# Optimization experiments

Measured on AMD Instinct MI355X. Metric: run time of the kernel, lower is better.

## Reference

```python
import jax, jax.numpy as jnp
import numpy as np
import math

B, DG, P, DA = 512, 1024, 1024, 256
LN_EPS = 1e-5  # torch LayerNorm default
EPS = 1e-12


def _ln(x, g, b):
    mu = jnp.mean(x, axis=-1, keepdims=True)
    var = jnp.mean((x - mu) ** 2, axis=-1, keepdims=True)
    return (x - mu) * jax.lax.rsqrt(var + LN_EPS) * g + b


def setup_inputs() -> dict:
    key = jax.random.key(0)
    ks = jax.random.split(key, 16)
    s = lambda fan_in: 1.0 / math.sqrt(fan_in)
    return {
        "hg": jax.random.normal(ks[0], (B, DG), jnp.float32),
        "desc_2d": jax.random.normal(ks[1], (B, P), jnp.float32),
        "Wq": jax.random.uniform(ks[2], (DA, DG), jnp.float32, -s(DG), s(DG)),
        "bq": jnp.zeros((DA,), jnp.float32),
        "wk_val": jax.random.uniform(ks[3], (DA,), jnp.float32, -1.0, 1.0),
        "bk_val": jax.random.uniform(ks[4], (DA,), jnp.float32, -1.0, 1.0),
        "wv_val": jax.random.uniform(ks[5], (DA,), jnp.float32, -1.0, 1.0),
        "bv_val": jax.random.uniform(ks[6], (DA,), jnp.float32, -1.0, 1.0),
        "Ek": jax.random.normal(ks[7], (P, DA), jnp.float32),
        "Ev": jax.random.normal(ks[8], (P, DA), jnp.float32),
        "Uq": jax.random.uniform(ks[9], (DA, DA), jnp.float32, -s(DA), s(DA)),
        "Vk": jax.random.uniform(ks[10], (DA, DA), jnp.float32, -s(DA), s(DA)),
        "ln_q_g": jnp.ones((DA,), jnp.float32), "ln_q_b": jnp.zeros((DA,), jnp.float32),
        "ln_k_g": jnp.ones((DA,), jnp.float32), "ln_k_b": jnp.zeros((DA,), jnp.float32),
        "ln_v_g": jnp.ones((DA,), jnp.float32), "ln_v_b": jnp.zeros((DA,), jnp.float32),
    }


def reference(hg, desc_2d, Wq, bq, wk_val, bk_val, wv_val, bv_val, Ek, Ev, Uq, Vk,
              ln_q_g, ln_q_b, ln_k_g, ln_k_b, ln_v_g, ln_v_b):
    # dropout is inference-mode (identity)
    q = _ln(hg @ Wq.T + bq, ln_q_g, ln_q_b)                       # (B, DA)
    # scalar -> token proj plus id embedding
    k = desc_2d[:, :, None] * wk_val + bk_val + Ek[None]          # (B, P, DA)
    v = desc_2d[:, :, None] * wv_val + bv_val + Ev[None]
    k = _ln(k, ln_k_g, ln_k_b)
    v = _ln(v, ln_v_g, ln_v_b)
    q2 = q @ Uq.T                                                 # (B, DA)
    k2 = jnp.einsum('bpd,ed->bpe', k, Vk)                         # (B, P, DA)
    e = jnp.einsum('bpd,bd->bp', k2, q2) / math.sqrt(DA)          # (B, P)
    alpha = jax.nn.sigmoid(e)
    alpha = alpha / (jnp.sum(alpha, axis=1, keepdims=True) + EPS)
    c = jnp.einsum('bp,bpd->bd', alpha, v)                        # (B, DA)
    return c, alpha
```

## Files before the change

### kernel.cpp

```cpp
#include <hip/hip_runtime.h>
#include <math.h>

#define B 512
#define DG 1024
#define P 1024
#define DA 256
#define LDP 68
#define BP (B * P)
#define BD (B * DA)

__device__ __forceinline__ float block_reduce_sum(float v, volatile float* red) {
    #pragma unroll
    for (int off = 32; off > 0; off >>= 1) v += __shfl_down(v, off, 64);
    const int lane = threadIdx.x & 63, wid = threadIdx.x >> 6;
    __syncthreads();
    if (lane == 0) red[wid] = v;
    __syncthreads();
    return red[0] + red[1] + red[2] + red[3];
}

__device__ __forceinline__ float wsum(float v) {
    #pragma unroll
    for (int m = 32; m > 0; m >>= 1) v += __shfl_xor(v, m, 64);
    return v;
}
__device__ __forceinline__ float txsum(float v) {
    #pragma unroll
    for (int m = 8; m > 0; m >>= 1) v += __shfl_xor(v, m, 16);
    return v;
}

#define FMA16(a4, b4, acc)                                   \
    acc[0][0] = fmaf(a4.x, b4.x, acc[0][0]);                 \
    acc[0][1] = fmaf(a4.x, b4.y, acc[0][1]);                 \
    acc[0][2] = fmaf(a4.x, b4.z, acc[0][2]);                 \
    acc[0][3] = fmaf(a4.x, b4.w, acc[0][3]);                 \
    acc[1][0] = fmaf(a4.y, b4.x, acc[1][0]);                 \
    acc[1][1] = fmaf(a4.y, b4.y, acc[1][1]);                 \
    acc[1][2] = fmaf(a4.y, b4.z, acc[1][2]);                 \
    acc[1][3] = fmaf(a4.y, b4.w, acc[1][3]);                 \
    acc[2][0] = fmaf(a4.z, b4.x, acc[2][0]);                 \
    acc[2][1] = fmaf(a4.z, b4.y, acc[2][1]);                 \
    acc[2][2] = fmaf(a4.z, b4.z, acc[2][2]);                 \
    acc[2][3] = fmaf(a4.z, b4.w, acc[2][3]);                 \
    acc[3][0] = fmaf(a4.w, b4.x, acc[3][0]);                 \
    acc[3][1] = fmaf(a4.w, b4.y, acc[3][1]);                 \
    acc[3][2] = fmaf(a4.w, b4.z, acc[3][2]);                 \
    acc[3][3] = fmaf(a4.w, b4.w, acc[3][3]);

#define FMA8(a0, a1, b4, acc)                                \
    acc[0][0] = fmaf(a0, b4.x, acc[0][0]);                   \
    acc[0][1] = fmaf(a0, b4.y, acc[0][1]);                   \
    acc[0][2] = fmaf(a0, b4.z, acc[0][2]);                   \
    acc[0][3] = fmaf(a0, b4.w, acc[0][3]);                   \
    acc[1][0] = fmaf(a1, b4.x, acc[1][0]);                   \
    acc[1][1] = fmaf(a1, b4.y, acc[1][1]);                   \
    acc[1][2] = fmaf(a1, b4.z, acc[1][2]);                   \
    acc[1][3] = fmaf(a1, b4.w, acc[1][3]);

__device__ __forceinline__ void stage_T(const float* __restrict__ src, int ldk, int m0, int k0,
                                        int tid, float* sD) {
    const int m = tid >> 3, k4 = (tid & 7) * 4;
    #pragma unroll
    for (int pass = 0; pass < 2; ++pass) {
        int mm = m + pass * 32;
        float4 v = *reinterpret_cast<const float4*>(&src[(m0 + mm) * ldk + k0 + k4]);
        sD[(k4 + 0) * LDP + mm] = v.x; sD[(k4 + 1) * LDP + mm] = v.y;
        sD[(k4 + 2) * LDP + mm] = v.z; sD[(k4 + 3) * LDP + mm] = v.w;
    }
}
__device__ __forceinline__ void stage_T32(const float* __restrict__ src, int ldk, int m0, int k0,
                                          int tid, float* sD) {
    const int m = tid >> 3, k4 = (tid & 7) * 4;
    float4 v = *reinterpret_cast<const float4*>(&src[(m0 + m) * ldk + k0 + k4]);
    sD[(k4 + 0) * LDP + m] = v.x; sD[(k4 + 1) * LDP + m] = v.y;
    sD[(k4 + 2) * LDP + m] = v.z; sD[(k4 + 3) * LDP + m] = v.w;
}
__device__ __forceinline__ void stage_N1(const float* __restrict__ src, int ldn, int k0, int n0,
                                         int tid, float* sD) {
    const int k = tid >> 4, n4 = (tid & 15) * 4;
    #pragma unroll
    for (int pass = 0; pass < 2; ++pass) {
        int kk = k + pass * 16;
        *reinterpret_cast<float4*>(&sD[kk * LDP + n4]) =
            *reinterpret_cast<const float4*>(&src[(k0 + kk) * ldn + n0 + n4]);
    }
}
__device__ __forceinline__ void stage_N4(const float* __restrict__ src, int pstride, int ldn,
                                         int k0, int n0, int tid, float* sD) {
    const int k = tid >> 4, n4 = (tid & 15) * 4;
    #pragma unroll
    for (int pass = 0; pass < 2; ++pass) {
        int kk = k + pass * 16;
        const float* base = &src[(k0 + kk) * ldn + n0 + n4];
        float4 v = *reinterpret_cast<const float4*>(base);
        #pragma unroll
        for (int s = 1; s < 4; ++s) {
            float4 w = *reinterpret_cast<const float4*>(base + s * pstride);
            v.x += w.x; v.y += w.y; v.z += w.z; v.w += w.w;
        }
        *reinterpret_cast<float4*>(&sD[kk * LDP + n4]) = v;
    }
}
__device__ __forceinline__ void mm_inner(const float* sA, const float* sB, int tid, float acc[4][4]) {
    const int ty4 = (tid >> 4) * 4, tx4 = (tid & 15) * 4;
    #pragma unroll
    for (int kk = 0; kk < 32; ++kk) {
        float4 a4 = *reinterpret_cast<const float4*>(&sA[kk * LDP + ty4]);
        float4 b4 = *reinterpret_cast<const float4*>(&sB[kk * LDP + tx4]);
        FMA16(a4, b4, acc)
    }
}

__global__ __launch_bounds__(256) void KA(const float* __restrict__ hg, const float* __restrict__ Wq,
                                          const float* __restrict__ Uq, const float* __restrict__ Vk,
                                          const float* __restrict__ Ek, const float* __restrict__ Ev,
                                          const float* __restrict__ wk, const float* __restrict__ bk,
                                          const float* __restrict__ wv, const float* __restrict__ bv,
                                          const float* __restrict__ gk, const float* __restrict__ bkln,
                                          float* __restrict__ qp, float* __restrict__ Gp,
                                          float* __restrict__ UqT, float* __restrict__ Sacc,
                                          float* __restrict__ pst, float* __restrict__ scal4,
                                          float* __restrict__ vec4) {
    __shared__ __align__(16) float sA[32 * LDP];
    __shared__ __align__(16) float sB[32 * LDP];
    const int tid = threadIdx.x;
    const int t = blockIdx.x;
    const int ty4 = (tid >> 4) * 4, tx4 = (tid & 15) * 4;

    if (t < 256) {
        const int mt = t & 7, nt = (t >> 3) & 3, ks = t >> 5;
        const int b0 = mt * 64, d0 = nt * 64, kc = ks * 128;
        float acc[4][4] = {};
        for (int kt = 0; kt < 128; kt += 32) {
            stage_T(hg, DG, b0, kc + kt, tid, sA);
            stage_T(Wq, DG, d0, kc + kt, tid, sB);
            __syncthreads();
            mm_inner(sA, sB, tid, acc);
            __syncthreads();
        }
        float* outp = qp + ks * BD;
        #pragma unroll
        for (int i = 0; i < 4; ++i) {
            float4 o = make_float4(acc[i][0], acc[i][1], acc[i][2], acc[i][3]);
            *reinterpret_cast<float4*>(&outp[(b0 + ty4 + i) * DA + d0 + tx4]) = o;
        }
    } else if (t < 512) {
        const int t2 = t - 256;
        const int et = t2 & 3, pt = (t2 >> 2) & 15, ks = t2 >> 6;
        const int e0 = et * 64, p0 = pt * 64, kc = ks * 64;
        float acc[4][4] = {};
        for (int kt = 0; kt < 64; kt += 32) {
            const int kg = kc + kt;
            {
                const int m = tid >> 3, k4 = (tid & 7) * 4;
                float4 g = *reinterpret_cast<const float4*>(&gk[kg + k4]);
                #pragma unroll
                for (int pass = 0; pass < 2; ++pass) {
                    int mm = m + pass * 32;
                    float4 v = *reinterpret_cast<const float4*>(&Vk[(e0 + mm) * DA + kg + k4]);
                    sA[(k4 + 0) * LDP + mm] = v.x * g.x; sA[(k4 + 1) * LDP + mm] = v.y * g.y;
                    sA[(k4 + 2) * LDP + mm] = v.z * g.z; sA[(k4 + 3) * LDP + mm] = v.w * g.w;
                }
            }
            stage_T(Ek, DA, p0, kg, tid, sB);
            __syncthreads();
            mm_inner(sA, sB, tid, acc);
            __syncthreads();
        }
        float* outp = Gp + ks * (DA * P);
        #pragma unroll
        for (int i = 0; i < 4; ++i) {
            float4 o = make_float4(acc[i][0], acc[i][1], acc[i][2], acc[i][3]);
            *reinterpret_cast<float4*>(&outp[(e0 + ty4 + i) * P + p0 + tx4]) = o;
        }
    } else if (t < 576) {
        const int b2 = t - 512;
        const int e0 = (b2 & 7) * 32, f0 = (b2 >> 3) * 32;
        const int col = tid & 31, row8 = tid >> 5;
        #pragma unroll
        for (int pass = 0; pass < 4; ++pass) {
            int r = row8 + pass * 8;
            sA[r * 33 + col] = Uq[(e0 + r) * DA + f0 + col];
        }
        __syncthreads();
        #pragma unroll
        for (int pass = 0; pass < 4; ++pass) {
            int r = row8 + pass * 8;
            UqT[(f0 + r) * DA + e0 + col] = sA[col * 33 + r];
        }
    } else if (t == 576) {
        #pragma unroll
        for (int j = 0; j < 8; ++j) Sacc[j * 256 + tid] = 0.f;
        float* w4  = sA;
        float* tmp = sB;
        float gkd = gk[tid];
        w4[0 * 256 + tid] = wk[tid] * gkd;
        w4[1 * 256 + tid] = bk[tid] * gkd;
        w4[2 * 256 + tid] = gkd;
        w4[3 * 256 + tid] = bkln[tid];
        __syncthreads();
        const int dl = tid & 15, eg = tid >> 4;
        for (int eb = 0; eb < 16; ++eb) {
            int e = eb * 16 + eg;
            float p0 = 0.f, p1 = 0.f, p2 = 0.f, p3 = 0.f;
            #pragma unroll
            for (int tt = 0; tt < 16; ++tt) {
                int d = dl + tt * 16;
                float v = Vk[e * DA + d];
                p0 = fmaf(v, w4[d], p0);
                p1 = fmaf(v, w4[256 + d], p1);
                p2 = fmaf(v, w4[512 + d], p2);
                p3 = fmaf(v, w4[768 + d], p3);
            }
            #pragma unroll
            for (int m = 8; m > 0; m >>= 1) {
                p0 += __shfl_xor(p0, m, 16);
                p1 += __shfl_xor(p1, m, 16);
                p2 += __shfl_xor(p2, m, 16);
                p3 += __shfl_xor(p3, m, 16);
            }
            if (dl == 0) {
                tmp[e * 4 + 0] = p0; tmp[e * 4 + 1] = p1;
                tmp[e * 4 + 2] = p2; tmp[e * 4 + 3] = p3;
            }
        }
        __syncthreads();
        float a0 = 0.f, a1 = 0.f, a2 = 0.f, a3 = 0.f;
        for (int e = 0; e < 256; ++e) {
            float u = Uq[e * DA + tid];
            a0 = fmaf(u, tmp[e * 4 + 0], a0);
            a1 = fmaf(u, tmp[e * 4 + 1], a1);
            a2 = fmaf(u, tmp[e * 4 + 2], a2);
            a3 = fmaf(u, tmp[e * 4 + 3], a3);
        }
        vec4[tid] = a0; vec4[256 + tid] = a1; vec4[512 + tid] = a2; vec4[768 + tid] = a3;
    } else {
        const int tp = t - 577;
        const int wid = tid >> 6, lane = tid & 63;
        const int p = tp * 4 + wid;
        const int d4 = lane * 4;
        const float inv = 1.0f / DA;
        float4 ek4 = *reinterpret_cast<const float4*>(&Ek[p * DA + d4]);
        float4 ev4 = *reinterpret_cast<const float4*>(&Ev[p * DA + d4]);
        float4 wk4 = *reinterpret_cast<const float4*>(&wk[d4]);
        float4 bk4 = *reinterpret_cast<const float4*>(&bk[d4]);
        float4 wv4 = *reinterpret_cast<const float4*>(&wv[d4]);
        float4 bv4 = *reinterpret_cast<const float4*>(&bv[d4]);
        float ck0 = bk4.x + ek4.x, ck1 = bk4.y + ek4.y, ck2 = bk4.z + ek4.z, ck3 = bk4.w + ek4.w;
        float cv0 = bv4.x + ev4.x, cv1 = bv4.y + ev4.y, cv2 = bv4.z + ev4.z, cv3 = bv4.w + ev4.w;
        float Sck  = wsum(ck0 + ck1 + ck2 + ck3);
        float Sck2 = wsum(ck0*ck0 + ck1*ck1 + ck2*ck2 + ck3*ck3);
        float Swck = wsum(wk4.x*ck0 + wk4.y*ck1 + wk4.z*ck2 + wk4.w*ck3);
        float Scv  = wsum(cv0 + cv1 + cv2 + cv3);
        float Scv2 = wsum(cv0*cv0 + cv1*cv1 + cv2*cv2 + cv3*cv3);
        float Swcv = wsum(wv4.x*cv0 + wv4.y*cv1 + wv4.z*cv2 + wv4.w*cv3);
        float Swk  = wsum(wk4.x + wk4.y + wk4.z + wk4.w);
        float Swv  = wsum(wv4.x + wv4.y + wv4.z + wv4.w);
        float mwk = Swk * inv, mwv = Swv * inv;
        float mck = Sck * inv, mcv = Scv * inv;
        if (lane == 0) {
            pst[0 * P + p] = mck;
            pst[1 * P + p] = Swck * inv - mwk * mck;
            pst[2 * P + p] = Sck2 * inv - mck * mck;
            pst[3 * P + p] = mcv;
            pst[4 * P + p] = Swcv * inv - mwv * mcv;
            pst[5 * P + p] = Scv2 * inv - mcv * mcv;
        }
        if (p == 0) {
            float Swk2 = wsum(wk4.x*wk4.x + wk4.y*wk4.y + wk4.z*wk4.z + wk4.w*wk4.w);
            float Swv2 = wsum(wv4.x*wv4.x + wv4.y*wv4.y + wv4.z*wv4.z + wv4.w*wv4.w);
            if (lane == 0) {
                scal4[0] = mwk;
                scal4[1] = Swk2 * inv - mwk * mwk;
                scal4[2] = mwv;
                scal4[3] = Swv2 * inv - mwv * mwv;
            }
        }
    }
}

__global__ __launch_bounds__(256) void KC(const float* __restrict__ qp, const float* __restrict__ bq,
                                          const float* __restrict__ gq, const float* __restrict__ bqln,
                                          const float* __restrict__ vec4, const float* __restrict__ UqT,
                                          float* __restrict__ q2out, float* __restrict__ bscal) {
    __shared__ __align__(16) float q_lds[DA];
    __shared__ float red[4];
    const int b = blockIdx.x, d = threadIdx.x;
    float x = bq[d];
    #pragma unroll
    for (int ks = 0; ks < 8; ++ks) x += qp[ks * BD + b * DA + d];
    float mu = block_reduce_sum(x, red) * (1.0f / DA);
    float xc = x - mu;
    float var = block_reduce_sum(xc * xc, red) * (1.0f / DA);
    float qv = xc * rsqrtf(var + 1e-5f) * gq[d] + bqln[d];
    q_lds[d] = qv;
    float Wg = block_reduce_sum(qv * vec4[d], red);
    float Cg = block_reduce_sum(qv * vec4[256 + d], red);
    float G_ = block_reduce_sum(qv * vec4[512 + d], red);
    float Bb = block_reduce_sum(qv * vec4[768 + d], red);
    if (d == 0) {
        bscal[b] = Wg; bscal[B + b] = Cg;
        bscal[2 * B + b] = G_; bscal[3 * B + b] = Bb;
    }
    float q2 = 0.f;
    for (int f = 0; f < DA; f += 4) {
        float4 qf = *reinterpret_cast<const float4*>(&q_lds[f]);
        q2 = fmaf(qf.x, UqT[(f + 0) * DA + d], q2);
        q2 = fmaf(qf.y, UqT[(f + 1) * DA + d], q2);
        q2 = fmaf(qf.z, UqT[(f + 2) * DA + d], q2);
        q2 = fmaf(qf.w, UqT[(f + 3) * DA + d], q2);
    }
    q2out[b * DA + d] = q2;
}

__global__ __launch_bounds__(256) void KD(const float* __restrict__ q2, const float* __restrict__ Gp,
                                          const float* __restrict__ desc, const float* __restrict__ bscal,
                                          const float* __restrict__ pst, const float* __restrict__ scal4,
                                          float* __restrict__ ubuf, float* __restrict__ wbuf,
                                          float* __restrict__ Sacc) {
    __shared__ __align__(16) float sA[32 * LDP];
    __shared__ __align__(16) float sB[32 * LDP];
    const int tid = threadIdx.x, t = blockIdx.x;
    const int tx = tid & 15, ty = tid >> 4;
    const int tx4 = tx * 4;
    const int b0 = (t & 15) * 32, p0 = (t >> 4) * 64;
    float acc[2][4] = {};
    for (int kt = 0; kt < 256; kt += 32) {
        stage_T32(q2, DA, b0, kt, tid, sA);
        stage_N4(Gp, DA * P, P, kt, p0, tid, sB);
        __syncthreads();
        #pragma unroll
        for (int kk = 0; kk < 32; ++kk) {
            float a0 = sA[kk * LDP + ty * 2 + 0];
            float a1 = sA[kk * LDP + ty * 2 + 1];
            float4 b4 = *reinterpret_cast<const float4*>(&sB[kk * LDP + tx4]);
            FMA8(a0, a1, b4, acc)
        }
        __syncthreads();
    }
    const float mwk = scal4[0], Ak = scal4[1], mwv = scal4[2], Av = scal4[3];
    #pragma unroll
    for (int i = 0; i < 2; ++i) {
        const int b = b0 + ty * 2 + i;
        const float Wg = bscal[b], Cg = bscal[B + b], G_ = bscal[2 * B + b], Bb = bscal[3 * B + b];
        float4 uo, wo;
        float* up = &uo.x; float* wp = &wo.x;
        float us = 0.f, ws_ = 0.f, wss = 0.f, wms = 0.f;
        #pragma unroll
        for (int j = 0; j < 4; ++j) {
            const int p = p0 + tx4 + j;
            float s = desc[b * P + p];
            float mck = pst[p], Bk = pst[P + p], Ck = pst[2 * P + p];
            float var = fmaf(s, fmaf(s, Ak, 2.0f * Bk), Ck);
            float rstd = rsqrtf(var + 1e-5f);
            float mu = fmaf(s, mwk, mck);
            float e = (rstd * (fmaf(s, Wg, Cg) + acc[i][j] - mu * G_) + Bb) * 0.0625f;
            float uu = 1.0f / (1.0f + expf(-e));
            float mcv = pst[3 * P + p], Bv = pst[4 * P + p], Cv = pst[5 * P + p];
            float varv = fmaf(s, fmaf(s, Av, 2.0f * Bv), Cv);
            float rv = rsqrtf(varv + 1e-5f);
            float ww = uu * rv;
            up[j] = uu; wp[j] = ww;
            us += uu; ws_ += ww;
            wss = fmaf(ww, s, wss);
            wms = fmaf(ww, fmaf(s, mwv, mcv), wms);
        }
        *reinterpret_cast<float4*>(&ubuf[b * P + p0 + tx4]) = uo;
        *reinterpret_cast<float4*>(&wbuf[b * P + p0 + tx4]) = wo;
        us = txsum(us); ws_ = txsum(ws_); wss = txsum(wss); wms = txsum(wms);
        if (tx == 0) {
            atomicAdd(&Sacc[b], us);
            atomicAdd(&Sacc[B + b], ws_);
            atomicAdd(&Sacc[2 * B + b], wss);
            atomicAdd(&Sacc[3 * B + b], wms);
        }
    }
}

__global__ __launch_bounds__(256) void KF(const float* __restrict__ wbuf, const float* __restrict__ Ev,
                                          float* __restrict__ cpart) {
    __shared__ __align__(16) float sA[32 * LDP];
    __shared__ __align__(16) float sB[32 * LDP];
    const int tid = threadIdx.x, t = blockIdx.x;
    const int ty4 = (tid >> 4) * 4, tx4 = (tid & 15) * 4;
    const int mt = t & 7, nt = (t >> 3) & 3, ks = t >> 5;
    const int b0 = mt * 64, d0 = nt * 64, kc = ks * 128;
    float acc[4][4] = {};
    for (int kt = 0; kt < 128; kt += 32) {
        stage_T(wbuf, P, b0, kc + kt, tid, sA);
        stage_N1(Ev, DA, kc + kt, d0, tid, sB);
        __syncthreads();
        mm_inner(sA, sB, tid, acc);
        __syncthreads();
    }
    float* outp = cpart + ks * BD;
    #pragma unroll
    for (int i = 0; i < 4; ++i) {
        float4 o = make_float4(acc[i][0], acc[i][1], acc[i][2], acc[i][3]);
        *reinterpret_cast<float4*>(&outp[(b0 + ty4 + i) * DA + d0 + tx4]) = o;
    }
}

__global__ __launch_bounds__(256) void KG(const float* __restrict__ cpart, const float* __restrict__ Sacc,
                                          const float* __restrict__ ubuf,
                                          const float* __restrict__ gv, const float* __restrict__ wv,
                                          const float* __restrict__ bvv, const float* __restrict__ bvln,
                                          float* __restrict__ alpha_out, float* __restrict__ out_c) {
    const int b = blockIdx.x, tid = threadIdx.x;
    const float S = Sacc[b], SB = Sacc[B + b], SBs = Sacc[2 * B + b], SBm = Sacc[3 * B + b];
    const float invS = 1.0f / (S + 1e-12f);
    const float T = S * invS;
    #pragma unroll
    for (int j = 0; j < 4; ++j) {
        int p = j * 256 + tid;
        alpha_out[b * P + p] = ubuf[b * P + p] * invS;
    }
    const int d = tid;
    float csum = 0.f;
    #pragma unroll
    for (int ks = 0; ks < 8; ++ks) csum += cpart[ks * BD + b * DA + d];
    out_c[b * DA + d] =
        invS * (gv[d] * (wv[d] * SBs + bvv[d] * SB + csum - SBm)) + bvln[d] * T;
}

extern "C" void kernel_launch(void* const* d_in, const int* in_sizes, int n_in,
                              void* d_out, int out_size, void* d_ws, size_t ws_size,
                              hipStream_t stream) {
    (void)in_sizes; (void)n_in; (void)out_size; (void)ws_size;
    const float* hg   = (const float*)d_in[0];
    const float* desc = (const float*)d_in[1];
    const float* Wq   = (const float*)d_in[2];
    const float* bq   = (const float*)d_in[3];
    const float* wk   = (const float*)d_in[4];
    const float* bk   = (const float*)d_in[5];
    const float* wv   = (const float*)d_in[6];
    const float* bv   = (const float*)d_in[7];
    const float* Ek   = (const float*)d_in[8];
    const float* Ev   = (const float*)d_in[9];
    const float* Uq   = (const float*)d_in[10];
    const float* Vk   = (const float*)d_in[11];
    const float* gq   = (const float*)d_in[12];
    const float* bqln = (const float*)d_in[13];
    const float* gk   = (const float*)d_in[14];
    const float* bkln = (const float*)d_in[15];
    const float* gv   = (const float*)d_in[16];
    const float* bvln = (const float*)d_in[17];

    float* out = (float*)d_out;
    float* out_c = out;
    float* out_alpha = out + BD;

    float* ws = (float*)d_ws;
    float* qp    = ws;
    float* Gp    = ws + 1048576;
    float* UqT   = ws + 2097152;
    float* q2    = ws + 2162688;
    float* ubuf  = ws + 2293760;
    float* wbuf  = ws + 2818048;
    float* cpart = ws + 3342336;
    float* vec4  = ws + 4390912;
    float* bscal = ws + 4391936;
    float* Sacc  = ws + 4393984;
    float* pst   = ws + 4396032;
    float* scal4 = ws + 4402176;

    KA<<<833, 256, 0, stream>>>(hg, Wq, Uq, Vk, Ek, Ev, wk, bk, wv, bv, gk, bkln,
                                qp, Gp, UqT, Sacc, pst, scal4, vec4);
    KC<<<512, 256, 0, stream>>>(qp, bq, gq, bqln, vec4, UqT, q2, bscal);
    KD<<<256, 256, 0, stream>>>(q2, Gp, desc, bscal, pst, scal4, ubuf, wbuf, Sacc);
    KF<<<256, 256, 0, stream>>>(wbuf, Ev, cpart);
    KG<<<512, 256, 0, stream>>>(cpart, Sacc, ubuf, gv, wv, bv, bvln, out_alpha, out_c);
}
```

Baseline: 70.31 us.

## Split-K the score GEMM, add per-row epilogue kernel, drop atomics

The Gp partials are reduced from four to two K-splits in KA. The score GEMM in KD becomes a 64x64-tiled split-K over four partial buffers instead of a 32-row tile with a fused sigmoid epilogue and atomics. A new per-row kernel KE sums the partials, applies the sigmoid and LayerNorm statistics, reduces the row sums in-block, and writes alpha and the bias part of c. KF now splits K into 16 chunks to raise block count, and KG only adds the GEMM term. This removes the Sacc zeroing and atomics and raises parallelism, at the cost of an extra launch and more partial-buffer traffic.

```diff
diff --git a/kernel.cpp b/kernel.cpp
--- a/kernel.cpp
+++ b/kernel.cpp
@@ -18,15 +18,9 @@
     __syncthreads();
     return red[0] + red[1] + red[2] + red[3];
 }
-
 __device__ __forceinline__ float wsum(float v) {
     #pragma unroll
     for (int m = 32; m > 0; m >>= 1) v += __shfl_xor(v, m, 64);
-    return v;
-}
-__device__ __forceinline__ float txsum(float v) {
-    #pragma unroll
-    for (int m = 8; m > 0; m >>= 1) v += __shfl_xor(v, m, 16);
     return v;
 }
 
@@ -48,16 +42,6 @@
     acc[3][2] = fmaf(a4.w, b4.z, acc[3][2]);                 \
     acc[3][3] = fmaf(a4.w, b4.w, acc[3][3]);
 
-#define FMA8(a0, a1, b4, acc)                                \
-    acc[0][0] = fmaf(a0, b4.x, acc[0][0]);                   \
-    acc[0][1] = fmaf(a0, b4.y, acc[0][1]);                   \
-    acc[0][2] = fmaf(a0, b4.z, acc[0][2]);                   \
-    acc[0][3] = fmaf(a0, b4.w, acc[0][3]);                   \
-    acc[1][0] = fmaf(a1, b4.x, acc[1][0]);                   \
-    acc[1][1] = fmaf(a1, b4.y, acc[1][1]);                   \
-    acc[1][2] = fmaf(a1, b4.z, acc[1][2]);                   \
-    acc[1][3] = fmaf(a1, b4.w, acc[1][3]);
-
 __device__ __forceinline__ void stage_T(const float* __restrict__ src, int ldk, int m0, int k0,
                                         int tid, float* sD) {
     const int m = tid >> 3, k4 = (tid & 7) * 4;
@@ -69,13 +53,6 @@
         sD[(k4 + 2) * LDP + mm] = v.z; sD[(k4 + 3) * LDP + mm] = v.w;
     }
 }
-__device__ __forceinline__ void stage_T32(const float* __restrict__ src, int ldk, int m0, int k0,
-                                          int tid, float* sD) {
-    const int m = tid >> 3, k4 = (tid & 7) * 4;
-    float4 v = *reinterpret_cast<const float4*>(&src[(m0 + m) * ldk + k0 + k4]);
-    sD[(k4 + 0) * LDP + m] = v.x; sD[(k4 + 1) * LDP + m] = v.y;
-    sD[(k4 + 2) * LDP + m] = v.z; sD[(k4 + 3) * LDP + m] = v.w;
-}
 __device__ __forceinline__ void stage_N1(const float* __restrict__ src, int ldn, int k0, int n0,
                                          int tid, float* sD) {
     const int k = tid >> 4, n4 = (tid & 15) * 4;
@@ -86,7 +63,7 @@
             *reinterpret_cast<const float4*>(&src[(k0 + kk) * ldn + n0 + n4]);
     }
 }
-__device__ __forceinline__ void stage_N4(const float* __restrict__ src, int pstride, int ldn,
+__device__ __forceinline__ void stage_N2(const float* __restrict__ src, int pstride, int ldn,
                                          int k0, int n0, int tid, float* sD) {
     const int k = tid >> 4, n4 = (tid & 15) * 4;
     #pragma unroll
@@ -94,11 +71,8 @@
         int kk = k + pass * 16;
         const float* base = &src[(k0 + kk) * ldn + n0 + n4];
         float4 v = *reinterpret_cast<const float4*>(base);
-        #pragma unroll
-        for (int s = 1; s < 4; ++s) {
-            float4 w = *reinterpret_cast<const float4*>(base + s * pstride);
-            v.x += w.x; v.y += w.y; v.z += w.z; v.w += w.w;
-        }
+        float4 w = *reinterpret_cast<const float4*>(base + pstride);
+        v.x += w.x; v.y += w.y; v.z += w.z; v.w += w.w;
         *reinterpret_cast<float4*>(&sD[kk * LDP + n4]) = v;
     }
 }
@@ -119,13 +93,12 @@
                                           const float* __restrict__ wv, const float* __restrict__ bv,
                                           const float* __restrict__ gk, const float* __restrict__ bkln,
                                           float* __restrict__ qp, float* __restrict__ Gp,
-                                          float* __restrict__ UqT, float* __restrict__ Sacc,
+                                          float* __restrict__ UqT,
                                           float* __restrict__ pst, float* __restrict__ scal4,
                                           float* __restrict__ vec4) {
     __shared__ __align__(16) float sA[32 * LDP];
     __shared__ __align__(16) float sB[32 * LDP];
-    const int tid = threadIdx.x;
-    const int t = blockIdx.x;
+    const int tid = threadIdx.x, t = blockIdx.x;
     const int ty4 = (tid >> 4) * 4, tx4 = (tid & 15) * 4;
 
     if (t < 256) {
@@ -145,12 +118,12 @@
             float4 o = make_float4(acc[i][0], acc[i][1], acc[i][2], acc[i][3]);
             *reinterpret_cast<float4*>(&outp[(b0 + ty4 + i) * DA + d0 + tx4]) = o;
         }
-    } else if (t < 512) {
+    } else if (t < 384) {
         const int t2 = t - 256;
         const int et = t2 & 3, pt = (t2 >> 2) & 15, ks = t2 >> 6;
-        const int e0 = et * 64, p0 = pt * 64, kc = ks * 64;
+        const int e0 = et * 64, p0 = pt * 64, kc = ks * 128;
         float acc[4][4] = {};
-        for (int kt = 0; kt < 64; kt += 32) {
+        for (int kt = 0; kt < 128; kt += 32) {
             const int kg = kc + kt;
             {
                 const int m = tid >> 3, k4 = (tid & 7) * 4;
@@ -174,8 +147,8 @@
             float4 o = make_float4(acc[i][0], acc[i][1], acc[i][2], acc[i][3]);
             *reinterpret_cast<float4*>(&outp[(e0 + ty4 + i) * P + p0 + tx4]) = o;
         }
-    } else if (t < 576) {
-        const int b2 = t - 512;
+    } else if (t < 448) {
+        const int b2 = t - 384;
         const int e0 = (b2 & 7) * 32, f0 = (b2 >> 3) * 32;
         const int col = tid & 31, row8 = tid >> 5;
         #pragma unroll
@@ -189,9 +162,7 @@
             int r = row8 + pass * 8;
             UqT[(f0 + r) * DA + e0 + col] = sA[col * 33 + r];
         }
-    } else if (t == 576) {
-        #pragma unroll
-        for (int j = 0; j < 8; ++j) Sacc[j * 256 + tid] = 0.f;
+    } else if (t == 448) {
         float* w4  = sA;
         float* tmp = sB;
         float gkd = gk[tid];
@@ -236,7 +207,7 @@
         }
         vec4[tid] = a0; vec4[256 + tid] = a1; vec4[512 + tid] = a2; vec4[768 + tid] = a3;
     } else {
-        const int tp = t - 577;
+        const int tp = t - 449;
         const int wid = tid >> 6, lane = tid & 63;
         const int p = tp * 4 + wid;
         const int d4 = lane * 4;
@@ -315,67 +286,76 @@
 }
 
 __global__ __launch_bounds__(256) void KD(const float* __restrict__ q2, const float* __restrict__ Gp,
-                                          const float* __restrict__ desc, const float* __restrict__ bscal,
-                                          const float* __restrict__ pst, const float* __restrict__ scal4,
-                                          float* __restrict__ ubuf, float* __restrict__ wbuf,
-                                          float* __restrict__ Sacc) {
+                                          float* __restrict__ epart) {
     __shared__ __align__(16) float sA[32 * LDP];
     __shared__ __align__(16) float sB[32 * LDP];
     const int tid = threadIdx.x, t = blockIdx.x;
-    const int tx = tid & 15, ty = tid >> 4;
-    const int tx4 = tx * 4;
-    const int b0 = (t & 15) * 32, p0 = (t >> 4) * 64;
-    float acc[2][4] = {};
-    for (int kt = 0; kt < 256; kt += 32) {
-        stage_T32(q2, DA, b0, kt, tid, sA);
-        stage_N4(Gp, DA * P, P, kt, p0, tid, sB);
-        __syncthreads();
-        #pragma unroll
-        for (int kk = 0; kk < 32; ++kk) {
-            float a0 = sA[kk * LDP + ty * 2 + 0];
-            float a1 = sA[kk * LDP + ty * 2 + 1];
-            float4 b4 = *reinterpret_cast<const float4*>(&sB[kk * LDP + tx4]);
-            FMA8(a0, a1, b4, acc)
-        }
-        __syncthreads();
-    }
+    const int ty4 = (tid >> 4) * 4, tx4 = (tid & 15) * 4;
+    const int bt = t & 7, pt = (t >> 3) & 15, ks = t >> 7;
+    const int b0 = bt * 64, p0 = pt * 64, kc = ks * 64;
+    float acc[4][4] = {};
+    for (int kt = 0; kt < 64; kt += 32) {
+        stage_T(q2, DA, b0, kc + kt, tid, sA);
+        stage_N2(Gp, DA * P, P, kc + kt, p0, tid, sB);
+        __syncthreads();
+        mm_inner(sA, sB, tid, acc);
+        __syncthreads();
+    }
+    float* outp = epart + ks * BP;
+    #pragma unroll
+    for (int i = 0; i < 4; ++i) {
+        float4 o = make_float4(acc[i][0], acc[i][1], acc[i][2], acc[i][3]);
+        *reinterpret_cast<float4*>(&outp[(b0 + ty4 + i) * P + p0 + tx4]) = o;
+    }
+}
+
+__global__ __launch_bounds__(256) void KE(const float* __restrict__ epart, const float* __restrict__ desc,
+                                          const float* __restrict__ bscal, const float* __restrict__ pst,
+                                          const float* __restrict__ scal4,
+                                          const float* __restrict__ gv, const float* __restrict__ wv,
+                                          const float* __restrict__ bvv, const float* __restrict__ bvln,
+                                          float* __restrict__ alpha_out, float* __restrict__ wbuf,
+                                          float* __restrict__ bscal2, float* __restrict__ out_c) {
+    __shared__ float red[4];
+    const int b = blockIdx.x, tid = threadIdx.x;
     const float mwk = scal4[0], Ak = scal4[1], mwv = scal4[2], Av = scal4[3];
-    #pragma unroll
-    for (int i = 0; i < 2; ++i) {
-        const int b = b0 + ty * 2 + i;
-        const float Wg = bscal[b], Cg = bscal[B + b], G_ = bscal[2 * B + b], Bb = bscal[3 * B + b];
-        float4 uo, wo;
-        float* up = &uo.x; float* wp = &wo.x;
-        float us = 0.f, ws_ = 0.f, wss = 0.f, wms = 0.f;
-        #pragma unroll
-        for (int j = 0; j < 4; ++j) {
-            const int p = p0 + tx4 + j;
-            float s = desc[b * P + p];
-            float mck = pst[p], Bk = pst[P + p], Ck = pst[2 * P + p];
-            float var = fmaf(s, fmaf(s, Ak, 2.0f * Bk), Ck);
-            float rstd = rsqrtf(var + 1e-5f);
-            float mu = fmaf(s, mwk, mck);
-            float e = (rstd * (fmaf(s, Wg, Cg) + acc[i][j] - mu * G_) + Bb) * 0.0625f;
-            float uu = 1.0f / (1.0f + expf(-e));
-            float mcv = pst[3 * P + p], Bv = pst[4 * P + p], Cv = pst[5 * P + p];
-            float varv = fmaf(s, fmaf(s, Av, 2.0f * Bv), Cv);
-            float rv = rsqrtf(varv + 1e-5f);
-            float ww = uu * rv;
-            up[j] = uu; wp[j] = ww;
-            us += uu; ws_ += ww;
-            wss = fmaf(ww, s, wss);
-            wms = fmaf(ww, fmaf(s, mwv, mcv), wms);
-        }
-        *reinterpret_cast<float4*>(&ubuf[b * P + p0 + tx4]) = uo;
-        *reinterpret_cast<float4*>(&wbuf[b * P + p0 + tx4]) = wo;
-        us = txsum(us); ws_ = txsum(ws_); wss = txsum(wss); wms = txsum(wms);
-        if (tx == 0) {
-            atomicAdd(&Sacc[b], us);
-            atomicAdd(&Sacc[B + b], ws_);
-            atomicAdd(&Sacc[2 * B + b], wss);
-            atomicAdd(&Sacc[3 * B + b], wms);
-        }
-    }
+    const float Wg = bscal[b], Cg = bscal[B + b], G_ = bscal[2 * B + b], Bb = bscal[3 * B + b];
+    float u[4];
+    float us = 0.f, ws_ = 0.f, wss = 0.f, wms = 0.f;
+    #pragma unroll
+    for (int j = 0; j < 4; ++j) {
+        int p = j * 256 + tid;
+        float dot = epart[b * P + p] + epart[BP + b * P + p]
+                  + epart[2 * BP + b * P + p] + epart[3 * BP + b * P + p];
+        float s = desc[b * P + p];
+        float mck = pst[p], Bk = pst[P + p], Ck = pst[2 * P + p];
+        float var = fmaf(s, fmaf(s, Ak, 2.0f * Bk), Ck);
+        float rstd = rsqrtf(var + 1e-5f);
+        float mu = fmaf(s, mwk, mck);
+        float e = (rstd * (fmaf(s, Wg, Cg) + dot - mu * G_) + Bb) * 0.0625f;
+        float uu = 1.0f / (1.0f + expf(-e));
+        float mcv = pst[3 * P + p], Bv = pst[4 * P + p], Cv = pst[5 * P + p];
+        float varv = fmaf(s, fmaf(s, Av, 2.0f * Bv), Cv);
+        float rv = rsqrtf(varv + 1e-5f);
+        float ww = uu * rv;
+        wbuf[b * P + p] = ww;
+        u[j] = uu;
+        us += uu; ws_ += ww;
+        wss = fmaf(ww, s, wss);
+        wms = fmaf(ww, fmaf(s, mwv, mcv), wms);
+    }
+    float S   = block_reduce_sum(us, red);
+    float SB  = block_reduce_sum(ws_, red);
+    float SBs = block_reduce_sum(wss, red);
+    float SBm = block_reduce_sum(wms, red);
+    float invS = 1.0f / (S + 1e-12f);
+    float T = S * invS;
+    #pragma unroll
+    for (int j = 0; j < 4; ++j)
+        alpha_out[b * P + j * 256 + tid] = u[j] * invS;
+    if (tid == 0) bscal2[b] = invS;
+    const int d = tid;
+    out_c[b * DA + d] = invS * (gv[d] * (wv[d] * SBs + bvv[d] * SB - SBm)) + bvln[d] * T;
 }
 
 __global__ __launch_bounds__(256) void KF(const float* __restrict__ wbuf, const float* __restrict__ Ev,
@@ -385,9 +365,9 @@
     const int tid = threadIdx.x, t = blockIdx.x;
     const int ty4 = (tid >> 4) * 4, tx4 = (tid & 15) * 4;
     const int mt = t & 7, nt = (t >> 3) & 3, ks = t >> 5;
-    const int b0 = mt * 64, d0 = nt * 64, kc = ks * 128;
+    const int b0 = mt * 64, d0 = nt * 64, kc = ks * 64;
     float acc[4][4] = {};
-    for (int kt = 0; kt < 128; kt += 32) {
+    for (int kt = 0; kt < 64; kt += 32) {
         stage_T(wbuf, P, b0, kc + kt, tid, sA);
         stage_N1(Ev, DA, kc + kt, d0, tid, sB);
         __syncthreads();
@@ -402,26 +382,13 @@
     }
 }
 
-__global__ __launch_bounds__(256) void KG(const float* __restrict__ cpart, const float* __restrict__ Sacc,
-                                          const float* __restrict__ ubuf,
-                                          const float* __restrict__ gv, const float* __restrict__ wv,
-                                          const float* __restrict__ bvv, const float* __restrict__ bvln,
-                                          float* __restrict__ alpha_out, float* __restrict__ out_c) {
-    const int b = blockIdx.x, tid = threadIdx.x;
-    const float S = Sacc[b], SB = Sacc[B + b], SBs = Sacc[2 * B + b], SBm = Sacc[3 * B + b];
-    const float invS = 1.0f / (S + 1e-12f);
-    const float T = S * invS;
-    #pragma unroll
-    for (int j = 0; j < 4; ++j) {
-        int p = j * 256 + tid;
-        alpha_out[b * P + p] = ubuf[b * P + p] * invS;
-    }
-    const int d = tid;
+__global__ __launch_bounds__(256) void KG(const float* __restrict__ cpart, const float* __restrict__ bscal2,
+                                          const float* __restrict__ gv, float* __restrict__ out_c) {
+    const int b = blockIdx.x, d = threadIdx.x;
     float csum = 0.f;
     #pragma unroll
-    for (int ks = 0; ks < 8; ++ks) csum += cpart[ks * BD + b * DA + d];
-    out_c[b * DA + d] =
-        invS * (gv[d] * (wv[d] * SBs + bvv[d] * SB + csum - SBm)) + bvln[d] * T;
+    for (int ks = 0; ks < 16; ++ks) csum += cpart[ks * BD + b * DA + d];
+    out_c[b * DA + d] = fmaf(bscal2[b] * gv[d], csum, out_c[b * DA + d]);
 }
 
 extern "C" void kernel_launch(void* const* d_in, const int* in_sizes, int n_in,
@@ -454,21 +421,23 @@
     float* ws = (float*)d_ws;
     float* qp    = ws;
     float* Gp    = ws + 1048576;
-    float* UqT   = ws + 2097152;
-    float* q2    = ws + 2162688;
-    float* ubuf  = ws + 2293760;
-    float* wbuf  = ws + 2818048;
-    float* cpart = ws + 3342336;
-    float* vec4  = ws + 4390912;
-    float* bscal = ws + 4391936;
-    float* Sacc  = ws + 4393984;
-    float* pst   = ws + 4396032;
-    float* scal4 = ws + 4402176;
-
-    KA<<<833, 256, 0, stream>>>(hg, Wq, Uq, Vk, Ek, Ev, wk, bk, wv, bv, gk, bkln,
-                                qp, Gp, UqT, Sacc, pst, scal4, vec4);
+    float* UqT   = ws + 1572864;
+    float* q2    = ws + 1638400;
+    float* epart = ws + 1769472;
+    float* wbuf  = ws + 3866624;
+    float* cpart = ws + 4390912;
+    float* vec4  = ws + 6488064;
+    float* bscal = ws + 6489088;
+    float* bscal2= ws + 6491136;
+    float* pst   = ws + 6491648;
+    float* scal4 = ws + 6497792;
+
+    KA<<<705, 256, 0, stream>>>(hg, Wq, Uq, Vk, Ek, Ev, wk, bk, wv, bv, gk, bkln,
+                                qp, Gp, UqT, pst, scal4, vec4);
     KC<<<512, 256, 0, stream>>>(qp, bq, gq, bqln, vec4, UqT, q2, bscal);
-    KD<<<256, 256, 0, stream>>>(q2, Gp, desc, bscal, pst, scal4, ubuf, wbuf, Sacc);
-    KF<<<256, 256, 0, stream>>>(wbuf, Ev, cpart);
-    KG<<<512, 256, 0, stream>>>(cpart, Sacc, ubuf, gv, wv, bv, bvln, out_alpha, out_c);
-}
+    KD<<<512, 256, 0, stream>>>(q2, Gp, epart);
+    KE<<<512, 256, 0, stream>>>(epart, desc, bscal, pst, scal4, gv, wv, bv, bvln,
+                                out_alpha, wbuf, bscal2, out_c);
+    KF<<<512, 256, 0, stream>>>(wbuf, Ev, cpart);
+    KG<<<512, 256, 0, stream>>>(cpart, bscal2, gv, out_c);
+}
```

New measurement: 64.05 us. 8.9% less time.

## Reassociate q·Uq·Vk·Ek via small M=Uq^T·diag(gk)Vk and fuse final reduction into KF

Applied to the files above, without the earlier changes.

Instead of precomputing G = (Vk·diag(gk))·Ek^T (DA×P, split-K partials summed in KD) and transposing Uq, the code precomputes the small DA×DA product M = Uq^T·diag(gk)·Vk in two split-K partials. KC then computes gr = q·M directly, and KD multiplies gr by Ek in place of summing four G partials. The separate KG kernel is removed: KF applies the normalisation epilogue and accumulates its split-K partials into out_c with atomicAdd (zeroed in KC), and also writes alpha. This cuts workspace traffic and one launch, at the cost of atomics and non-deterministic summation order.

```diff
diff --git a/kernel.cpp b/kernel.cpp
--- a/kernel.cpp
+++ b/kernel.cpp
@@ -18,7 +18,6 @@
     __syncthreads();
     return red[0] + red[1] + red[2] + red[3];
 }
-
 __device__ __forceinline__ float wsum(float v) {
     #pragma unroll
     for (int m = 32; m > 0; m >>= 1) v += __shfl_xor(v, m, 64);
@@ -86,22 +85,6 @@
             *reinterpret_cast<const float4*>(&src[(k0 + kk) * ldn + n0 + n4]);
     }
 }
-__device__ __forceinline__ void stage_N4(const float* __restrict__ src, int pstride, int ldn,
-                                         int k0, int n0, int tid, float* sD) {
-    const int k = tid >> 4, n4 = (tid & 15) * 4;
-    #pragma unroll
-    for (int pass = 0; pass < 2; ++pass) {
-        int kk = k + pass * 16;
-        const float* base = &src[(k0 + kk) * ldn + n0 + n4];
-        float4 v = *reinterpret_cast<const float4*>(base);
-        #pragma unroll
-        for (int s = 1; s < 4; ++s) {
-            float4 w = *reinterpret_cast<const float4*>(base + s * pstride);
-            v.x += w.x; v.y += w.y; v.z += w.z; v.w += w.w;
-        }
-        *reinterpret_cast<float4*>(&sD[kk * LDP + n4]) = v;
-    }
-}
 __device__ __forceinline__ void mm_inner(const float* sA, const float* sB, int tid, float acc[4][4]) {
     const int ty4 = (tid >> 4) * 4, tx4 = (tid & 15) * 4;
     #pragma unroll
@@ -118,14 +101,13 @@
                                           const float* __restrict__ wk, const float* __restrict__ bk,
                                           const float* __restrict__ wv, const float* __restrict__ bv,
                                           const float* __restrict__ gk, const float* __restrict__ bkln,
-                                          float* __restrict__ qp, float* __restrict__ Gp,
-                                          float* __restrict__ UqT, float* __restrict__ Sacc,
+                                          float* __restrict__ qp, float* __restrict__ Mp,
+                                          float* __restrict__ Sacc,
                                           float* __restrict__ pst, float* __restrict__ scal4,
                                           float* __restrict__ vec4) {
     __shared__ __align__(16) float sA[32 * LDP];
     __shared__ __align__(16) float sB[32 * LDP];
-    const int tid = threadIdx.x;
-    const int t = blockIdx.x;
+    const int tid = threadIdx.x, t = blockIdx.x;
     const int ty4 = (tid >> 4) * 4, tx4 = (tid & 15) * 4;
 
     if (t < 256) {
@@ -145,51 +127,34 @@
             float4 o = make_float4(acc[i][0], acc[i][1], acc[i][2], acc[i][3]);
             *reinterpret_cast<float4*>(&outp[(b0 + ty4 + i) * DA + d0 + tx4]) = o;
         }
-    } else if (t < 512) {
+    } else if (t < 288) {
         const int t2 = t - 256;
-        const int et = t2 & 3, pt = (t2 >> 2) & 15, ks = t2 >> 6;
-        const int e0 = et * 64, p0 = pt * 64, kc = ks * 64;
+        const int ft = t2 & 3, dt = (t2 >> 2) & 3, ks = t2 >> 4;
+        const int f0 = ft * 64, d0 = dt * 64, kc = ks * 128;
+        const int k = tid >> 4, n4 = (tid & 15) * 4;
         float acc[4][4] = {};
-        for (int kt = 0; kt < 64; kt += 32) {
+        for (int kt = 0; kt < 128; kt += 32) {
             const int kg = kc + kt;
-            {
-                const int m = tid >> 3, k4 = (tid & 7) * 4;
-                float4 g = *reinterpret_cast<const float4*>(&gk[kg + k4]);
-                #pragma unroll
-                for (int pass = 0; pass < 2; ++pass) {
-                    int mm = m + pass * 32;
-                    float4 v = *reinterpret_cast<const float4*>(&Vk[(e0 + mm) * DA + kg + k4]);
-                    sA[(k4 + 0) * LDP + mm] = v.x * g.x; sA[(k4 + 1) * LDP + mm] = v.y * g.y;
-                    sA[(k4 + 2) * LDP + mm] = v.z * g.z; sA[(k4 + 3) * LDP + mm] = v.w * g.w;
-                }
+            stage_N1(Uq, DA, kg, f0, tid, sA);
+            float4 g = *reinterpret_cast<const float4*>(&gk[d0 + n4]);
+            #pragma unroll
+            for (int pass = 0; pass < 2; ++pass) {
+                int kk = k + pass * 16;
+                float4 v = *reinterpret_cast<const float4*>(&Vk[(kg + kk) * DA + d0 + n4]);
+                v.x *= g.x; v.y *= g.y; v.z *= g.z; v.w *= g.w;
+                *reinterpret_cast<float4*>(&sB[kk * LDP + n4]) = v;
             }
-            stage_T(Ek, DA, p0, kg, tid, sB);
             __syncthreads();
             mm_inner(sA, sB, tid, acc);
             __syncthreads();
         }
-        float* outp = Gp + ks * (DA * P);
+        float* outp = Mp + ks * (DA * DA);
         #pragma unroll
         for (int i = 0; i < 4; ++i) {
             float4 o = make_float4(acc[i][0], acc[i][1], acc[i][2], acc[i][3]);
-            *reinterpret_cast<float4*>(&outp[(e0 + ty4 + i) * P + p0 + tx4]) = o;
-        }
-    } else if (t < 576) {
-        const int b2 = t - 512;
-        const int e0 = (b2 & 7) * 32, f0 = (b2 >> 3) * 32;
-        const int col = tid & 31, row8 = tid >> 5;
-        #pragma unroll
-        for (int pass = 0; pass < 4; ++pass) {
-            int r = row8 + pass * 8;
-            sA[r * 33 + col] = Uq[(e0 + r) * DA + f0 + col];
-        }
-        __syncthreads();
-        #pragma unroll
-        for (int pass = 0; pass < 4; ++pass) {
-            int r = row8 + pass * 8;
-            UqT[(f0 + r) * DA + e0 + col] = sA[col * 33 + r];
-        }
-    } else if (t == 576) {
+            *reinterpret_cast<float4*>(&outp[(f0 + ty4 + i) * DA + d0 + tx4]) = o;
+        }
+    } else if (t == 288) {
         #pragma unroll
         for (int j = 0; j < 8; ++j) Sacc[j * 256 + tid] = 0.f;
         float* w4  = sA;
@@ -236,7 +201,7 @@
         }
         vec4[tid] = a0; vec4[256 + tid] = a1; vec4[512 + tid] = a2; vec4[768 + tid] = a3;
     } else {
-        const int tp = t - 577;
+        const int tp = t - 289;
         const int wid = tid >> 6, lane = tid & 63;
         const int p = tp * 4 + wid;
         const int d4 = lane * 4;
@@ -282,8 +247,9 @@
 
 __global__ __launch_bounds__(256) void KC(const float* __restrict__ qp, const float* __restrict__ bq,
                                           const float* __restrict__ gq, const float* __restrict__ bqln,
-                                          const float* __restrict__ vec4, const float* __restrict__ UqT,
-                                          float* __restrict__ q2out, float* __restrict__ bscal) {
+                                          const float* __restrict__ vec4, const float* __restrict__ Mp,
+                                          float* __restrict__ gr, float* __restrict__ bscal,
+                                          float* __restrict__ out_c) {
     __shared__ __align__(16) float q_lds[DA];
     __shared__ float red[4];
     const int b = blockIdx.x, d = threadIdx.x;
@@ -303,18 +269,21 @@
         bscal[b] = Wg; bscal[B + b] = Cg;
         bscal[2 * B + b] = G_; bscal[3 * B + b] = Bb;
     }
-    float q2 = 0.f;
+    out_c[b * DA + d] = 0.f;
+    const float* M0 = Mp;
+    const float* M1 = Mp + DA * DA;
+    float grv = 0.f;
     for (int f = 0; f < DA; f += 4) {
         float4 qf = *reinterpret_cast<const float4*>(&q_lds[f]);
-        q2 = fmaf(qf.x, UqT[(f + 0) * DA + d], q2);
-        q2 = fmaf(qf.y, UqT[(f + 1) * DA + d], q2);
-        q2 = fmaf(qf.z, UqT[(f + 2) * DA + d], q2);
-        q2 = fmaf(qf.w, UqT[(f + 3) * DA + d], q2);
-    }
-    q2out[b * DA + d] = q2;
-}
-
-__global__ __launch_bounds__(256) void KD(const float* __restrict__ q2, const float* __restrict__ Gp,
+        grv = fmaf(qf.x, M0[(f + 0) * DA + d] + M1[(f + 0) * DA + d], grv);
+        grv = fmaf(qf.y, M0[(f + 1) * DA + d] + M1[(f + 1) * DA + d], grv);
+        grv = fmaf(qf.z, M0[(f + 2) * DA + d] + M1[(f + 2) * DA + d], grv);
+        grv = fmaf(qf.w, M0[(f + 3) * DA + d] + M1[(f + 3) * DA + d], grv);
+    }
+    gr[b * DA + d] = grv;
+}
+
+__global__ __launch_bounds__(256) void KD(const float* __restrict__ gr, const float* __restrict__ Ek,
                                           const float* __restrict__ desc, const float* __restrict__ bscal,
                                           const float* __restrict__ pst, const float* __restrict__ scal4,
                                           float* __restrict__ ubuf, float* __restrict__ wbuf,
@@ -327,8 +296,8 @@
     const int b0 = (t & 15) * 32, p0 = (t >> 4) * 64;
     float acc[2][4] = {};
     for (int kt = 0; kt < 256; kt += 32) {
-        stage_T32(q2, DA, b0, kt, tid, sA);
-        stage_N4(Gp, DA * P, P, kt, p0, tid, sB);
+        stage_T32(gr, DA, b0, kt, tid, sA);
+        stage_T(Ek, DA, p0, kt, tid, sB);
         __syncthreads();
         #pragma unroll
         for (int kk = 0; kk < 32; ++kk) {
@@ -378,8 +347,11 @@
     }
 }
 
-__global__ __launch_bounds__(256) void KF(const float* __restrict__ wbuf, const float* __restrict__ Ev,
-                                          float* __restrict__ cpart) {
+__global__ __launch_bounds__(256) void KF(const float* __restrict__ ubuf, const float* __restrict__ wbuf,
+                                          const float* __restrict__ Ev, const float* __restrict__ Sacc,
+                                          const float* __restrict__ gv, const float* __restrict__ wv,
+                                          const float* __restrict__ bvv, const float* __restrict__ bvln,
+                                          float* __restrict__ out_c, float* __restrict__ alpha_out) {
     __shared__ __align__(16) float sA[32 * LDP];
     __shared__ __align__(16) float sB[32 * LDP];
     const int tid = threadIdx.x, t = blockIdx.x;
@@ -394,34 +366,42 @@
         mm_inner(sA, sB, tid, acc);
         __syncthreads();
     }
-    float* outp = cpart + ks * BD;
+    float4 g4 = *reinterpret_cast<const float4*>(&gv[d0 + tx4]);
+    float4 wv4 = *reinterpret_cast<const float4*>(&wv[d0 + tx4]);
+    float4 bv4 = *reinterpret_cast<const float4*>(&bvv[d0 + tx4]);
+    float4 bl4 = *reinterpret_cast<const float4*>(&bvln[d0 + tx4]);
     #pragma unroll
     for (int i = 0; i < 4; ++i) {
-        float4 o = make_float4(acc[i][0], acc[i][1], acc[i][2], acc[i][3]);
-        *reinterpret_cast<float4*>(&outp[(b0 + ty4 + i) * DA + d0 + tx4]) = o;
-    }
-}
-
-__global__ __launch_bounds__(256) void KG(const float* __restrict__ cpart, const float* __restrict__ Sacc,
-                                          const float* __restrict__ ubuf,
-                                          const float* __restrict__ gv, const float* __restrict__ wv,
-                                          const float* __restrict__ bvv, const float* __restrict__ bvln,
-                                          float* __restrict__ alpha_out, float* __restrict__ out_c) {
-    const int b = blockIdx.x, tid = threadIdx.x;
-    const float S = Sacc[b], SB = Sacc[B + b], SBs = Sacc[2 * B + b], SBm = Sacc[3 * B + b];
-    const float invS = 1.0f / (S + 1e-12f);
-    const float T = S * invS;
-    #pragma unroll
-    for (int j = 0; j < 4; ++j) {
-        int p = j * 256 + tid;
-        alpha_out[b * P + p] = ubuf[b * P + p] * invS;
-    }
-    const int d = tid;
-    float csum = 0.f;
-    #pragma unroll
-    for (int ks = 0; ks < 8; ++ks) csum += cpart[ks * BD + b * DA + d];
-    out_c[b * DA + d] =
-        invS * (gv[d] * (wv[d] * SBs + bvv[d] * SB + csum - SBm)) + bvln[d] * T;
+        const int b = b0 + ty4 + i;
+        const float S = Sacc[b], SB = Sacc[B + b], SBs = Sacc[2 * B + b], SBm = Sacc[3 * B + b];
+        const float invS = 1.0f / (S + 1e-12f);
+        float v0 = acc[i][0] * invS * g4.x;
+        float v1 = acc[i][1] * invS * g4.y;
+        float v2 = acc[i][2] * invS * g4.z;
+        float v3 = acc[i][3] * invS * g4.w;
+        if (ks == 0) {
+            const float T = S * invS;
+            v0 += invS * g4.x * (wv4.x * SBs + bv4.x * SB - SBm) + bl4.x * T;
+            v1 += invS * g4.y * (wv4.y * SBs + bv4.y * SB - SBm) + bl4.y * T;
+            v2 += invS * g4.z * (wv4.z * SBs + bv4.z * SB - SBm) + bl4.z * T;
+            v3 += invS * g4.w * (wv4.w * SBs + bv4.w * SB - SBm) + bl4.w * T;
+        }
+        float* dst = &out_c[b * DA + d0 + tx4];
+        atomicAdd(dst + 0, v0);
+        atomicAdd(dst + 1, v1);
+        atomicAdd(dst + 2, v2);
+        atomicAdd(dst + 3, v3);
+    }
+    if (nt == 0) {
+        #pragma unroll
+        for (int r = 0; r < 32; ++r) {
+            int idx = r * 256 + tid;
+            int b = b0 + (idx >> 7);
+            int p = kc + (idx & 127);
+            float S = Sacc[b];
+            alpha_out[b * P + p] = ubuf[b * P + p] / (S + 1e-12f);
+        }
+    }
 }
 
 extern "C" void kernel_launch(void* const* d_in, const int* in_sizes, int n_in,
@@ -453,22 +433,19 @@
 
     float* ws = (float*)d_ws;
     float* qp    = ws;
-    float* Gp    = ws + 1048576;
-    float* UqT   = ws + 2097152;
-    float* q2    = ws + 2162688;
-    float* ubuf  = ws + 2293760;
-    float* wbuf  = ws + 2818048;
-    float* cpart = ws + 3342336;
-    float* vec4  = ws + 4390912;
-    float* bscal = ws + 4391936;
-    float* Sacc  = ws + 4393984;
-    float* pst   = ws + 4396032;
-    float* scal4 = ws + 4402176;
-
-    KA<<<833, 256, 0, stream>>>(hg, Wq, Uq, Vk, Ek, Ev, wk, bk, wv, bv, gk, bkln,
-                                qp, Gp, UqT, Sacc, pst, scal4, vec4);
-    KC<<<512, 256, 0, stream>>>(qp, bq, gq, bqln, vec4, UqT, q2, bscal);
-    KD<<<256, 256, 0, stream>>>(q2, Gp, desc, bscal, pst, scal4, ubuf, wbuf, Sacc);
-    KF<<<256, 256, 0, stream>>>(wbuf, Ev, cpart);
-    KG<<<512, 256, 0, stream>>>(cpart, Sacc, ubuf, gv, wv, bv, bvln, out_alpha, out_c);
-}
+    float* Mp    = ws + 1048576;
+    float* gr    = ws + 1179648;
+    float* ubuf  = ws + 1310720;
+    float* wbuf  = ws + 1835008;
+    float* vec4  = ws + 2359296;
+    float* bscal = ws + 2360320;
+    float* Sacc  = ws + 2362368;
+    float* pst   = ws + 2364416;
+    float* scal4 = ws + 2370560;
+
+    KA<<<545, 256, 0, stream>>>(hg, Wq, Uq, Vk, Ek, Ev, wk, bk, wv, bv, gk, bkln,
+                                qp, Mp, Sacc, pst, scal4, vec4);
+    KC<<<512, 256, 0, stream>>>(qp, bq, gq, bqln, vec4, Mp, gr, bscal, out_c);
+    KD<<<256, 256, 0, stream>>>(gr, Ek, desc, bscal, pst, scal4, ubuf, wbuf, Sacc);
+    KF<<<256, 256, 0, stream>>>(ubuf, wbuf, Ev, Sacc, gv, wv, bv, bvln, out_c, out_alpha);
+}
```

New measurement: 83.65 us. 19.0% more time.
